# Optimization experiments

Hardware: AMD Instinct MI355X
Metric: run time of the kernel (lower is better)

Reference implementation:

```python
import jax, jax.numpy as jnp
import numpy as np

B, P, ENC = 128, 196, 2048
A, E, D, V, L = 512, 512, 512, 10000, 22


def setup_inputs() -> dict:
    key = jax.random.key(0)
    ks = jax.random.split(key, 24)
    rn = lambda k, shp, s=0.02: jax.random.normal(k, shp, dtype=jnp.float32) * s
    lengths = jnp.sort(jax.random.randint(ks[3], (B,), 2, L + 1))[::-1]
    lengths = lengths.at[0].set(L)  # ensure max_len = L-1 decode steps
    return {
        "encoder_out": jax.random.normal(ks[0], (B, P, ENC), dtype=jnp.float32),
        "encoded_captions": jax.random.randint(ks[1], (B, L), 0, V),
        "caption_lengths": lengths,
        "E_emb": rn(ks[2], (V, E)),
        "W_enc_att": rn(ks[4], (A, ENC)), "b_enc_att": jnp.zeros((A,), jnp.float32),
        "W_dec_att": rn(ks[5], (A, D)), "b_dec_att": jnp.zeros((A,), jnp.float32),
        "w_full": rn(ks[6], (1, A)), "b_full": jnp.zeros((1,), jnp.float32),
        "W_init_h": rn(ks[7], (D, ENC)), "b_init_h": jnp.zeros((D,), jnp.float32),
        "W_init_c": rn(ks[8], (D, ENC)), "b_init_c": jnp.zeros((D,), jnp.float32),
        "W_ih": rn(ks[9], (4 * D, E + ENC)), "b_ih": jnp.zeros((4 * D,), jnp.float32),
        "W_hh": rn(ks[10], (4 * D, D)), "b_hh": jnp.zeros((4 * D,), jnp.float32),
        "W_fc": rn(ks[11], (V, D)), "b_fc": jnp.zeros((V,), jnp.float32),
    }


def reference(encoder_out, encoded_captions, caption_lengths, E_emb,
              W_enc_att, b_enc_att, W_dec_att, b_dec_att, w_full, b_full,
              W_init_h, b_init_h, W_init_c, b_init_c,
              W_ih, b_ih, W_hh, b_hh, W_fc, b_fc):
    T = encoded_captions.shape[1] - 1  # max decode steps (static)
    dec_len = caption_lengths - 1
    mean_enc = encoder_out.mean(axis=1)  # [B, ENC]
    h0 = mean_enc @ W_init_h.T + b_init_h
    c0 = mean_enc @ W_init_c.T + b_init_c
    # encoder-side attention projection is constant across timesteps -> hoist
    att1 = jnp.einsum('bpe,ae->bpa', encoder_out, W_enc_att) + b_enc_att  # [B,P,A]
    embs = E_emb[encoded_captions]  # [B, L, E]

    def step(carry, xs):
        h, c = carry
        t, emb_t = xs  # emb_t: [B, E]
        att2 = h @ W_dec_att.T + b_dec_att  # [B, A]
        e = jnp.einsum('bpa,a->bp', jax.nn.relu(att1 + att2[:, None, :]), w_full[0]) + b_full[0]
        alpha = jax.nn.softmax(e, axis=1)  # [B, P]
        awe = jnp.einsum('bpe,bp->be', encoder_out, alpha)  # [B, ENC]
        x = jnp.concatenate([emb_t, awe], axis=1)  # [B, E+ENC]
        gates = x @ W_ih.T + b_ih + h @ W_hh.T + b_hh  # [B, 4D]
        i, f, g, o = jnp.split(gates, 4, axis=1)
        i, f, o = jax.nn.sigmoid(i), jax.nn.sigmoid(f), jax.nn.sigmoid(o)
        g = jnp.tanh(g)
        c_new = f * c + i * g
        h_new = o * jnp.tanh(c_new)
        active = (dec_len > t)[:, None]  # ragged trim -> mask
        h2 = jnp.where(active, h_new, h)
        c2 = jnp.where(active, c_new, c)
        pred = jnp.where(active, h_new @ W_fc.T + b_fc, 0.0)  # [B, V]
        al = jnp.where(active, alpha, 0.0)
        return (h2, c2), (pred, al)

    xs = (jnp.arange(T), jnp.swapaxes(embs[:, :T], 0, 1))
    (_, _), (preds, alphas) = jax.lax.scan(step, (h0, c0), xs)
    return jnp.swapaxes(preds, 0, 1), jnp.swapaxes(alphas, 0, 1)
```

## Files before the change

kernel.cpp:

```cpp
#include <hip/hip_runtime.h>
#include <hip/hip_bf16.h>

#define B_  128
#define P_  196
#define ENCD 2048
#define A_  512
#define E_  512
#define D_  512
#define V_  10000
#define L_  22
#define T_  21
#define VPAD 10112

typedef __attribute__((ext_vector_type(8))) short short8;
typedef __attribute__((ext_vector_type(4))) float f32x4;

static __device__ __forceinline__ float bf2f(unsigned short u){
  union { unsigned int i; float f; } x; x.i = ((unsigned int)u) << 16; return x.f;
}
static __device__ __forceinline__ unsigned short f2bf(float f){
  union { float f; unsigned int i; } x; x.f = f;
  unsigned int r = x.i + 0x7fffu + ((x.i >> 16) & 1u);
  return (unsigned short)(r >> 16);
}
static __device__ __forceinline__ unsigned int pack2(float a, float b){
  return (unsigned int)f2bf(a) | ((unsigned int)f2bf(b) << 16);
}
static __device__ __forceinline__ void glds16(const void* g, void* l){
  __builtin_amdgcn_global_load_lds((const __attribute__((address_space(1))) void*)g,
                                   (__attribute__((address_space(3))) void*)l, 16, 0, 0);
}

__global__ __launch_bounds__(256) void gemm128(
    const unsigned short* __restrict__ A, int lda,
    const unsigned short* __restrict__ B, int ldb, int K,
    const float* __restrict__ bias,
    float* __restrict__ outF, long ldo,
    unsigned short* __restrict__ outB, long ldob,
    int ntiles)
{
  __shared__ unsigned short As[2][128*32];
  __shared__ unsigned short Bs[2][128*32];
  int bid = blockIdx.x, nblk = gridDim.x;
  if ((nblk & 7) == 0){ int per = nblk >> 3; bid = (bid & 7)*per + (bid >> 3); }
  int nt = bid % ntiles, mt = bid / ntiles;
  int tid = threadIdx.x, wave = tid >> 6, lane = tid & 63;
  int quad = lane >> 4, l16 = lane & 15;

  const unsigned short* ga = A + (size_t)(mt*128 + wave*32 + (lane>>2))*lda + (lane&3)*8;
  const unsigned short* gb = B + (size_t)(nt*128 + wave*32 + (lane>>2))*ldb + (lane&3)*8;

  int wm = wave >> 1, wn = wave & 1;

  auto STAGE = [&](int buf, int kk){
    unsigned short* la = &As[buf][wave*1024];
    unsigned short* lb = &Bs[buf][wave*1024];
    glds16(ga + kk,                  la);
    glds16(ga + kk + (size_t)16*lda, la + 512);
    glds16(gb + kk,                  lb);
    glds16(gb + kk + (size_t)16*ldb, lb + 512);
  };

  f32x4 acc[4][4];
  #pragma unroll
  for (int i=0;i<4;++i)
    #pragma unroll
    for (int j=0;j<4;++j) acc[i][j] = (f32x4){0.f,0.f,0.f,0.f};

  STAGE(0, 0);
  int cur = 0;
  for (int k=0; k<K; k+=32){
    __syncthreads();
    if (k+32 < K) STAGE(cur^1, k+32);
    const unsigned short* rA = &As[cur][(wm*64 + l16)*32 + quad*8];
    const unsigned short* rB = &Bs[cur][(wn*64 + l16)*32 + quad*8];
    short8 af[4], bfr[4];
    #pragma unroll
    for (int i=0;i<4;++i) af[i]  = *(const short8*)(rA + i*16*32);
    #pragma unroll
    for (int i=0;i<4;++i) bfr[i] = *(const short8*)(rB + i*16*32);
    #pragma unroll
    for (int mf=0;mf<4;++mf)
      #pragma unroll
      for (int nf=0;nf<4;++nf)
        acc[mf][nf] = __builtin_amdgcn_mfma_f32_16x16x32_bf16(af[mf], bfr[nf], acc[mf][nf], 0,0,0);
    cur ^= 1;
  }

  #pragma unroll
  for (int mf=0;mf<4;++mf){
    long mbase = mt*128 + wm*64 + mf*16 + quad*4;
    #pragma unroll
    for (int nf=0;nf<4;++nf){
      int col = nt*128 + wn*64 + nf*16 + l16;
      float bv = bias ? bias[col] : 0.f;
      #pragma unroll
      for (int r=0;r<4;++r){
        float v = acc[mf][nf][r] + bv;
        long m = mbase + r;
        if (outF) outF[m*ldo + col] = v;
        if (outB) outB[m*ldob + col] = f2bf(v);
      }
    }
  }
}

__global__ __launch_bounds__(256) void gemm_preds(
    const unsigned short* __restrict__ A,
    const unsigned short* __restrict__ B,
    const float* __restrict__ bias,
    const int* __restrict__ rs,
    const int* __restrict__ trow, const int* __restrict__ brow,
    float* __restrict__ out)
{
  __shared__ unsigned short As[2][128*32];
  __shared__ unsigned short Bs[2][128*32];
  int nt = blockIdx.x % 79, mt = blockIdx.x / 79;
  int NR = rs[T_];
  if (mt*128 >= NR) return;
  int tid = threadIdx.x, wave = tid >> 6, lane = tid & 63;
  int quad = lane >> 4, l16 = lane & 15;

  const unsigned short* ga = A + (size_t)(mt*128 + wave*32 + (lane>>2))*D_ + (lane&3)*8;
  const unsigned short* gb = B + (size_t)(nt*128 + wave*32 + (lane>>2))*D_ + (lane&3)*8;

  int wm = wave >> 1, wn = wave & 1;

  auto STAGE = [&](int buf, int kk){
    unsigned short* la = &As[buf][wave*1024];
    unsigned short* lb = &Bs[buf][wave*1024];
    glds16(ga + kk,                 la);
    glds16(ga + kk + (size_t)16*D_, la + 512);
    glds16(gb + kk,                 lb);
    glds16(gb + kk + (size_t)16*D_, lb + 512);
  };

  f32x4 acc[4][4];
  #pragma unroll
  for (int i=0;i<4;++i)
    #pragma unroll
    for (int j=0;j<4;++j) acc[i][j] = (f32x4){0.f,0.f,0.f,0.f};

  STAGE(0, 0);
  int cur = 0;
  for (int k=0; k<D_; k+=32){
    __syncthreads();
    if (k+32 < D_) STAGE(cur^1, k+32);
    const unsigned short* rA = &As[cur][(wm*64 + l16)*32 + quad*8];
    const unsigned short* rB = &Bs[cur][(wn*64 + l16)*32 + quad*8];
    short8 af[4], bfr[4];
    #pragma unroll
    for (int i=0;i<4;++i) af[i]  = *(const short8*)(rA + i*16*32);
    #pragma unroll
    for (int i=0;i<4;++i) bfr[i] = *(const short8*)(rB + i*16*32);
    #pragma unroll
    for (int mf=0;mf<4;++mf)
      #pragma unroll
      for (int nf=0;nf<4;++nf)
        acc[mf][nf] = __builtin_amdgcn_mfma_f32_16x16x32_bf16(af[mf], bfr[nf], acc[mf][nf], 0,0,0);
    cur ^= 1;
  }

  #pragma unroll
  for (int mf=0;mf<4;++mf){
    int mbase = mt*128 + wm*64 + mf*16 + quad*4;
    #pragma unroll
    for (int nf=0;nf<4;++nf){
      int col = nt*128 + wn*64 + nf*16 + l16;
      if (col >= V_) continue;
      float bv = bias[col];
      #pragma unroll
      for (int r=0;r<4;++r){
        int row = mbase + r;
        if (row >= NR) continue;
        int tt = trow[row], bb = brow[row];
        out[(size_t)(bb*T_ + tt)*V_ + col] = acc[mf][nf][r] + bv;
      }
    }
  }
}

__global__ __launch_bounds__(512) void att_step(
    const float* __restrict__ h,
    const unsigned short* __restrict__ WdaT,
    const float* __restrict__ bda,
    const unsigned short* __restrict__ att1,
    const float* __restrict__ wfull, const float* __restrict__ bfull,
    const unsigned short* __restrict__ enc_bf,
    const int* __restrict__ actv, int t,
    unsigned short* __restrict__ awe_bf,
    float* __restrict__ out_alpha, long ldo)
{
  __shared__ float hs[D_];
  __shared__ float att2p[1024];
  __shared__ float att2s[A_];
  __shared__ float wfs[A_];
  __shared__ float als[256];
  __shared__ float red[16];

  int bid = blockIdx.x, tid = threadIdx.x;
  int wave = tid >> 6, lane = tid & 63;
  int b = bid >> 1, j = bid & 1;

  if (b >= actv[t]){
    if (j == 0 && tid < P_) out_alpha[(size_t)b*ldo + tid] = 0.f;
    return;
  }

  if (tid < 128){
    ((float4*)wfs)[tid] = ((const float4*)wfull)[tid];
    ((float4*)hs)[tid]  = ((const float4*)(h + (size_t)b*D_))[tid];
  }
  __syncthreads();

  {
    int half = tid >> 8, ap = tid & 255;
    const unsigned int* wp = (const unsigned int*)WdaT + (size_t)half*256*256 + ap;
    const float* hh = hs + half*256;
    float s0 = 0.f, s1 = 0.f;
    #pragma unroll 4
    for (int k=0;k<256;++k){
      unsigned int v = wp[(size_t)k*256];
      float hk = hh[k];
      s0 = fmaf(bf2f((unsigned short)(v & 0xffffu)), hk, s0);
      s1 = fmaf(bf2f((unsigned short)(v >> 16)),     hk, s1);
    }
    att2p[half*512 + ap*2]     = s0;
    att2p[half*512 + ap*2 + 1] = s1;
  }
  __syncthreads();
  if (tid < A_) att2s[tid] = att2p[tid] + att2p[512 + tid] + bda[tid];
  __syncthreads();

  for (int p = wave; p < P_; p += 8){
    short8 v = *(const short8*)(att1 + ((size_t)(b*P_ + p))*A_ + lane*8);
    float4 a20 = *(const float4*)(att2s + lane*8);
    float4 a21 = *(const float4*)(att2s + lane*8 + 4);
    float4 wf0 = *(const float4*)(wfs + lane*8);
    float4 wf1 = *(const float4*)(wfs + lane*8 + 4);
    float s = 0.f;
    s += fmaxf(bf2f((unsigned short)v[0]) + a20.x, 0.f) * wf0.x;
    s += fmaxf(bf2f((unsigned short)v[1]) + a20.y, 0.f) * wf0.y;
    s += fmaxf(bf2f((unsigned short)v[2]) + a20.z, 0.f) * wf0.z;
    s += fmaxf(bf2f((unsigned short)v[3]) + a20.w, 0.f) * wf0.w;
    s += fmaxf(bf2f((unsigned short)v[4]) + a21.x, 0.f) * wf1.x;
    s += fmaxf(bf2f((unsigned short)v[5]) + a21.y, 0.f) * wf1.y;
    s += fmaxf(bf2f((unsigned short)v[6]) + a21.z, 0.f) * wf1.z;
    s += fmaxf(bf2f((unsigned short)v[7]) + a21.w, 0.f) * wf1.w;
    #pragma unroll
    for (int off=32; off; off>>=1) s += __shfl_xor(s, off, 64);
    if (lane == 0) als[p] = s + bfull[0];
  }
  __syncthreads();

  float ev = (tid < P_) ? als[tid] : -1e30f;
  float mx = ev;
  #pragma unroll
  for (int off=32; off; off>>=1) mx = fmaxf(mx, __shfl_xor(mx, off, 64));
  if (lane == 0) red[wave] = mx;
  __syncthreads();
  float bmax = fmaxf(fmaxf(fmaxf(red[0],red[1]), fmaxf(red[2],red[3])),
                     fmaxf(fmaxf(red[4],red[5]), fmaxf(red[6],red[7])));
  float ex = (tid < P_) ? __expf(ev - bmax) : 0.f;
  float sm = ex;
  #pragma unroll
  for (int off=32; off; off>>=1) sm += __shfl_xor(sm, off, 64);
  if (lane == 0) red[8 + wave] = sm;
  __syncthreads();
  float inv = 1.f / (red[8]+red[9]+red[10]+red[11]+red[12]+red[13]+red[14]+red[15]);
  if (tid < P_){
    float alpha = ex * inv;
    als[tid] = alpha;
    if (j == 0) out_alpha[(size_t)b*ldo + tid] = alpha;
  }
  __syncthreads();

  {
    int cu = j*512 + tid;
    const unsigned int* ep = (const unsigned int*)enc_bf + (size_t)b*P_*1024 + cu;
    float a0 = 0.f, a1 = 0.f;
    for (int p=0; p<P_; p+=2){
      unsigned int v0 = ep[(size_t)(p+0)*1024];
      unsigned int v1 = ep[(size_t)(p+1)*1024];
      float x0 = als[p], x1 = als[p+1];
      a0 = fmaf(bf2f((unsigned short)(v0 & 0xffffu)), x0, a0);
      a1 = fmaf(bf2f((unsigned short)(v0 >> 16)),     x0, a1);
      a0 = fmaf(bf2f((unsigned short)(v1 & 0xffffu)), x1, a0);
      a1 = fmaf(bf2f((unsigned short)(v1 >> 16)),     x1, a1);
    }
    ((unsigned int*)awe_bf)[(size_t)b*1024 + cu] = pack2(a0, a1);
  }
}

__global__ __launch_bounds__(512) void gates_step(
    const unsigned short* __restrict__ hbf,
    const unsigned short* __restrict__ Whh,
    const unsigned short* __restrict__ awe,
    const unsigned short* __restrict__ Wienc,
    const float* __restrict__ gates_pre,
    float* __restrict__ h, float* __restrict__ c,
    unsigned short* __restrict__ hbf_out,
    unsigned short* __restrict__ h_cmp,
    const int* __restrict__ lens,
    const int* __restrict__ actv, const int* __restrict__ rs, int t)
{
  __shared__ float reds[8*1024];
  int bid = blockIdx.x;
  int nt = (bid & 7)*4 + ((bid >> 3) & 3);
  int mt = bid >> 5;
  int tid = threadIdx.x, wave = tid >> 6, lane = tid & 63;
  int quad = lane >> 4, l16 = lane & 15;
  int m0 = mt*16;
  int nact = actv[t];

  if (m0 >= nact){
    if (tid < 256){
      int mi = tid >> 4, di = tid & 15;
      int idx = (m0 + mi)*512 + nt*16 + di;
      hbf_out[idx] = hbf[idx];
    }
    return;
  }

  int ks = wave*320, ke = ks + 320;
  f32x4 acc[4];
  #pragma unroll
  for (int f=0;f<4;++f) acc[f] = (f32x4){0.f,0.f,0.f,0.f};

  for (int kk=ks; kk<ke; kk+=32){
    const unsigned short* Ap; const unsigned short* Bp; int k, lda2, ldb2;
    if (kk < 512){ Ap = hbf;  Bp = Whh;   k = kk;       lda2 = 512;  ldb2 = 512;  }
    else         { Ap = awe;  Bp = Wienc; k = kk - 512; lda2 = 2048; ldb2 = 2048; }
    short8 a = *(const short8*)(Ap + (size_t)(m0 + l16)*lda2 + k + quad*8);
    #pragma unroll
    for (int f=0;f<4;++f){
      short8 bb = *(const short8*)(Bp + (size_t)(nt*16 + f*512 + l16)*ldb2 + k + quad*8);
      acc[f] = __builtin_amdgcn_mfma_f32_16x16x32_bf16(a, bb, acc[f], 0,0,0);
    }
  }
  {
    float* dst = &reds[wave*1024 + lane*16];
    #pragma unroll
    for (int f=0;f<4;++f) ((f32x4*)dst)[f] = acc[f];
  }
  __syncthreads();
  if (tid < 256){
    int mi = tid >> 4, di = tid & 15;
    int m = m0 + mi, d = nt*16 + di;
    int rl = ((mi>>2)*16 + di)*16 + (mi&3);
    float g4[4];
    #pragma unroll
    for (int f=0;f<4;++f){
      float s = 0.f;
      #pragma unroll
      for (int w=0;w<8;++w) s += reds[w*1024 + rl + f*4];
      g4[f] = s;
    }
    const float* gp = gates_pre + ((size_t)m*T_ + t)*2048;
    float vi = g4[0] + gp[d];
    float vf = g4[1] + gp[512 + d];
    float vg = g4[2] + gp[1024 + d];
    float vo = g4[3] + gp[1536 + d];
    float si = 1.f/(1.f + __expf(-vi));
    float sf = 1.f/(1.f + __expf(-vf));
    float so = 1.f/(1.f + __expf(-vo));
    float tg = tanhf(vg);
    int idx = m*512 + d;
    float cn = sf*c[idx] + si*tg;
    float hn = so*tanhf(cn);
    bool act = m < nact;
    float h2 = act ? hn : h[idx];
    float c2 = act ? cn : c[idx];
    h[idx] = h2; c[idx] = c2;
    unsigned short hb = f2bf(h2);
    hbf_out[idx] = hb;
    if (act) h_cmp[(size_t)(rs[t] + m)*512 + d] = hb;
  }
}

__global__ __launch_bounds__(256) void calc_active(
    const int* __restrict__ lens, int* __restrict__ actv,
    int* __restrict__ rs, int* __restrict__ trow, int* __restrict__ brow)
{
  __shared__ int scnt[T_];
  __shared__ int srs[T_+1];
  int tid = threadIdx.x;
  if (tid < T_){
    int cnt = 0;
    for (int b=0;b<B_;++b) cnt += ((lens[b]-1) > tid) ? 1 : 0;
    scnt[tid] = cnt; actv[tid] = cnt;
  }
  __syncthreads();
  if (tid == 0){
    int s = 0;
    for (int t=0;t<T_;++t){ srs[t] = s; rs[t] = s; s += scnt[t]; }
    srs[T_] = s; rs[T_] = s;
  }
  __syncthreads();
  int NR = srs[T_];
  for (int r = tid; r < NR; r += 256){
    int t = 0;
    while (r >= srs[t+1]) ++t;
    trow[r] = t; brow[r] = r - srs[t];
  }
}

__global__ __launch_bounds__(256) void zero_inactive(
    const int* __restrict__ lens, float* __restrict__ out)
{
  int bid = blockIdx.x;
  int b = bid / T_, t = bid - b*T_;
  if ((lens[b]-1) > t) return;
  float4* o = (float4*)(out + (size_t)(b*T_ + t)*V_);
  float4 z = {0.f,0.f,0.f,0.f};
  for (int i = threadIdx.x; i < V_/4; i += 256) o[i] = z;
}

__global__ __launch_bounds__(256) void enc_cvt_mean(
    const float* __restrict__ enc, unsigned short* __restrict__ enc_bf,
    unsigned short* __restrict__ mean_bf)
{
  int b = blockIdx.x >> 1;
  int c = (blockIdx.x & 1)*1024 + threadIdx.x*4;
  size_t base = (size_t)b*P_*ENCD + c;
  float s0=0.f,s1=0.f,s2=0.f,s3=0.f;
  for (int p=0; p<P_; p+=2){
    float4 v0 = *(const float4*)(enc + base + (size_t)(p+0)*ENCD);
    float4 v1 = *(const float4*)(enc + base + (size_t)(p+1)*ENCD);
    s0 += v0.x + v1.x; s1 += v0.y + v1.y; s2 += v0.z + v1.z; s3 += v0.w + v1.w;
    uint2 r0; r0.x = pack2(v0.x, v0.y); r0.y = pack2(v0.z, v0.w);
    uint2 r1; r1.x = pack2(v1.x, v1.y); r1.y = pack2(v1.z, v1.w);
    *(uint2*)(enc_bf + base + (size_t)(p+0)*ENCD) = r0;
    *(uint2*)(enc_bf + base + (size_t)(p+1)*ENCD) = r1;
  }
  const float is = 1.f/196.f;
  uint2 m; m.x = pack2(s0*is, s1*is); m.y = pack2(s2*is, s3*is);
  *(uint2*)(mean_bf + (size_t)b*ENCD + c) = m;
}

__global__ __launch_bounds__(256) void cvt_bf16(
    const float* __restrict__ in, unsigned short* __restrict__ out, int n4)
{
  int i = blockIdx.x*256 + threadIdx.x;
  if (i < n4){
    float4 v = ((const float4*)in)[i];
    uint2 o; o.x = pack2(v.x, v.y); o.y = pack2(v.z, v.w);
    ((uint2*)out)[i] = o;
  }
}

__global__ __launch_bounds__(256) void cvt_T_512(
    const float* __restrict__ W, unsigned short* __restrict__ WT)
{
  int a = blockIdx.x;
  for (int k = threadIdx.x; k < 512; k += 256)
    WT[(size_t)k*512 + a] = f2bf(W[(size_t)a*512 + k]);
}

__global__ __launch_bounds__(256) void split_wih(
    const float* __restrict__ W, unsigned short* __restrict__ Wemb,
    unsigned short* __restrict__ Wenc)
{
  int j = blockIdx.x;
  for (int k4 = threadIdx.x; k4 < 640; k4 += 256){
    float4 v = *(const float4*)(W + (size_t)j*2560 + k4*4);
    uint2 o; o.x = pack2(v.x, v.y); o.y = pack2(v.z, v.w);
    if (k4 < 128) *(uint2*)(Wemb + (size_t)j*512  + k4*4)        = o;
    else          *(uint2*)(Wenc + (size_t)j*2048 + (k4-128)*4)  = o;
  }
}

__global__ void add_bias2(const float* __restrict__ a, const float* __restrict__ b,
                          float* __restrict__ out, int n)
{
  int i = blockIdx.x*256 + threadIdx.x;
  if (i < n) out[i] = a[i] + b[i];
}

__global__ __launch_bounds__(128) void gather_emb(
    const int* __restrict__ caps, const float* __restrict__ E,
    unsigned short* __restrict__ X)
{
  int r = blockIdx.x;
  int b = r / T_, t = r - b*T_;
  int tok = caps[b*L_ + t];
  int c = threadIdx.x*4;
  float4 v = *(const float4*)(E + (size_t)tok*E_ + c);
  uint2 o; o.x = pack2(v.x, v.y); o.y = pack2(v.z, v.w);
  *(uint2*)(X + (size_t)r*E_ + c) = o;
}

extern "C" void kernel_launch(void* const* d_in, const int* in_sizes, int n_in,
                              void* d_out, int out_size, void* d_ws, size_t ws_size,
                              hipStream_t stream)
{
  const float* enc   = (const float*)d_in[0];
  const int*   caps  = (const int*)d_in[1];
  const int*   lens  = (const int*)d_in[2];
  const float* Eemb  = (const float*)d_in[3];
  const float* Wea   = (const float*)d_in[4];
  const float* bea   = (const float*)d_in[5];
  const float* Wda   = (const float*)d_in[6];
  const float* bda   = (const float*)d_in[7];
  const float* wfull = (const float*)d_in[8];
  const float* bfull = (const float*)d_in[9];
  const float* Wih0  = (const float*)d_in[10];
  const float* bih0  = (const float*)d_in[11];
  const float* Wic0  = (const float*)d_in[12];
  const float* bic0  = (const float*)d_in[13];
  const float* Wih   = (const float*)d_in[14];
  const float* bih   = (const float*)d_in[15];
  const float* Whh   = (const float*)d_in[16];
  const float* bhh   = (const float*)d_in[17];
  const float* Wfc   = (const float*)d_in[18];
  const float* bfc   = (const float*)d_in[19];

  char* wsp = (char*)d_ws;
  auto carve = [&](size_t bytes) -> char* {
    char* p = wsp; wsp += (bytes + 255) & ~(size_t)255; return p;
  };
  unsigned short* enc_bf   = (unsigned short*)carve((size_t)B_*P_*ENCD*2);
  unsigned short* att1_bf  = (unsigned short*)carve((size_t)B_*P_*A_*2);
  unsigned short* mean_bf  = (unsigned short*)carve((size_t)B_*ENCD*2);
  float*          gates_pre= (float*)carve((size_t)B_*T_*2048*4);
  unsigned short* X_emb    = (unsigned short*)carve((size_t)B_*T_*E_*2);
  unsigned short* Wea_bf   = (unsigned short*)carve((size_t)A_*ENCD*2);
  unsigned short* WdaT_bf  = (unsigned short*)carve((size_t)A_*D_*2);
  unsigned short* Wh0_bf   = (unsigned short*)carve((size_t)D_*ENCD*2);
  unsigned short* Wc0_bf   = (unsigned short*)carve((size_t)D_*ENCD*2);
  unsigned short* Whh_bf   = (unsigned short*)carve((size_t)2048*D_*2);
  unsigned short* Wie_bf   = (unsigned short*)carve((size_t)2048*E_*2);
  unsigned short* Wienc_bf = (unsigned short*)carve((size_t)2048*ENCD*2);
  unsigned short* Wfc_bf   = (unsigned short*)carve((size_t)VPAD*D_*2);
  float*          bias_ifgo= (float*)carve((size_t)2048*4);
  float*          h        = (float*)carve((size_t)B_*D_*4);
  float*          c        = (float*)carve((size_t)B_*D_*4);
  unsigned short* h_bf_all = (unsigned short*)carve((size_t)(T_+1)*B_*D_*2);
  unsigned short* h_cmp    = (unsigned short*)carve((size_t)T_*B_*D_*2);
  unsigned short* awe_bf   = (unsigned short*)carve((size_t)B_*ENCD*2);
  int*            actv     = (int*)carve(64*4);
  int*            rs       = (int*)carve(64*4);
  int*            trow     = (int*)carve((size_t)T_*B_*4);
  int*            brow     = (int*)carve((size_t)T_*B_*4);

  float* out_preds  = (float*)d_out;
  float* out_alphas = (float*)d_out + (size_t)B_*T_*V_;

  calc_active<<<1, 256, 0, stream>>>(lens, actv, rs, trow, brow);
  zero_inactive<<<B_*T_, 256, 0, stream>>>(lens, out_preds);
  enc_cvt_mean<<<256, 256, 0, stream>>>(enc, enc_bf, mean_bf);
  cvt_bf16<<<1024, 256, 0, stream>>>(Wea,  Wea_bf, A_*ENCD/4);
  cvt_T_512<<<512, 256, 0, stream>>>(Wda, WdaT_bf);
  cvt_bf16<<<1024, 256, 0, stream>>>(Wih0, Wh0_bf, D_*ENCD/4);
  cvt_bf16<<<1024, 256, 0, stream>>>(Wic0, Wc0_bf, D_*ENCD/4);
  cvt_bf16<<<1024, 256, 0, stream>>>(Whh,  Whh_bf, 2048*D_/4);
  cvt_bf16<<<5000, 256, 0, stream>>>(Wfc,  Wfc_bf, V_*D_/4);
  split_wih<<<2048, 256, 0, stream>>>(Wih, Wie_bf, Wienc_bf);
  add_bias2<<<8, 256, 0, stream>>>(bih, bhh, bias_ifgo, 2048);
  gather_emb<<<B_*T_, 128, 0, stream>>>(caps, Eemb, X_emb);

  gemm128<<<1*4, 256, 0, stream>>>(mean_bf, ENCD, Wh0_bf, ENCD, ENCD,
                                   bih0, h, D_, h_bf_all, D_, 4);
  gemm128<<<1*4, 256, 0, stream>>>(mean_bf, ENCD, Wc0_bf, ENCD, ENCD,
                                   bic0, c, D_, (unsigned short*)0, 0, 4);
  gemm128<<<196*4, 256, 0, stream>>>(enc_bf, ENCD, Wea_bf, ENCD, ENCD,
                                     bea, (float*)0, 0, att1_bf, A_, 4);
  gemm128<<<21*16, 256, 0, stream>>>(X_emb, E_, Wie_bf, E_, E_,
                                     bias_ifgo, gates_pre, 2048, (unsigned short*)0, 0, 16);

  for (int t = 0; t < T_; ++t){
    att_step<<<2*B_, 512, 0, stream>>>(h, WdaT_bf, bda, att1_bf, wfull, bfull,
                                       enc_bf, actv, t, awe_bf,
                                       out_alphas + (size_t)t*P_, (long)T_*P_);
    gates_step<<<256, 512, 0, stream>>>(h_bf_all + (size_t)t*B_*D_, Whh_bf,
                                        awe_bf, Wienc_bf, gates_pre,
                                        h, c, h_bf_all + (size_t)(t+1)*B_*D_,
                                        h_cmp, lens, actv, rs, t);
  }

  gemm_preds<<<21*79, 256, 0, stream>>>(h_cmp, Wfc_bf, bfc, rs, trow, brow,
                                        out_preds);
}
```

Measured before the change: 1.954 ms.

## Fuse per-step attention and gate kernels into one persistent kernel with grid barriers

Replaces the 42 per-timestep launches of att_step and gates_step with a single persistent kernel of 256 blocks. The blocks loop over timesteps and use an atomic-counter grid barrier between the attention phase and the gate phase. This removes kernel launch overhead and inter-kernel gaps. It relies on all 256 blocks being co-resident, since the barrier deadlocks otherwise. It also adds spin-wait cost and a larger shared-memory footprint per block, which may lower occupancy.

```diff
diff --git a/kernel.cpp b/kernel.cpp
--- a/kernel.cpp
+++ b/kernel.cpp
@@ -11,6 +11,7 @@
 #define L_  22
 #define T_  21
 #define VPAD 10112
+#define NBLK 256
 
 typedef __attribute__((ext_vector_type(8))) short short8;
 typedef __attribute__((ext_vector_type(4))) float f32x4;
@@ -29,6 +30,18 @@
 static __device__ __forceinline__ void glds16(const void* g, void* l){
   __builtin_amdgcn_global_load_lds((const __attribute__((address_space(1))) void*)g,
                                    (__attribute__((address_space(3))) void*)l, 16, 0, 0);
+}
+
+static __device__ __forceinline__ void gridbar(int* cnt, int target){
+  __syncthreads();
+  if (threadIdx.x == 0){
+    __threadfence();
+    __hip_atomic_fetch_add(cnt, 1, __ATOMIC_ACQ_REL, __HIP_MEMORY_SCOPE_AGENT);
+    while (__hip_atomic_load(cnt, __ATOMIC_ACQUIRE, __HIP_MEMORY_SCOPE_AGENT) < target)
+      __builtin_amdgcn_s_sleep(2);
+    __threadfence();
+  }
+  __syncthreads();
 }
 
 __global__ __launch_bounds__(256) void gemm128(
@@ -180,16 +193,23 @@
   }
 }
 
-__global__ __launch_bounds__(512) void att_step(
-    const float* __restrict__ h,
+__global__ __launch_bounds__(512) void decode_persist(
+    float* __restrict__ h,
     const unsigned short* __restrict__ WdaT,
     const float* __restrict__ bda,
     const unsigned short* __restrict__ att1,
     const float* __restrict__ wfull, const float* __restrict__ bfull,
     const unsigned short* __restrict__ enc_bf,
-    const int* __restrict__ actv, int t,
+    const unsigned short* __restrict__ Whh,
+    const unsigned short* __restrict__ Wienc,
+    const float* __restrict__ gates_pre,
+    float* __restrict__ c,
+    unsigned short* __restrict__ h_bf_all,
+    unsigned short* __restrict__ h_cmp,
     unsigned short* __restrict__ awe_bf,
-    float* __restrict__ out_alpha, long ldo)
+    const int* __restrict__ actv, const int* __restrict__ rs,
+    float* __restrict__ out_alphas,
+    int* __restrict__ barcnt)
 {
   __shared__ float hs[D_];
   __shared__ float att2p[1024];
@@ -197,194 +217,191 @@
   __shared__ float wfs[A_];
   __shared__ float als[256];
   __shared__ float red[16];
+  __shared__ float reds[8*1024];
 
   int bid = blockIdx.x, tid = threadIdx.x;
   int wave = tid >> 6, lane = tid & 63;
+  int quad = lane >> 4, l16 = lane & 15;
   int b = bid >> 1, j = bid & 1;
-
-  if (b >= actv[t]){
-    if (j == 0 && tid < P_) out_alpha[(size_t)b*ldo + tid] = 0.f;
-    return;
-  }
-
-  if (tid < 128){
-    ((float4*)wfs)[tid] = ((const float4*)wfull)[tid];
-    ((float4*)hs)[tid]  = ((const float4*)(h + (size_t)b*D_))[tid];
-  }
-  __syncthreads();
-
-  {
-    int half = tid >> 8, ap = tid & 255;
-    const unsigned int* wp = (const unsigned int*)WdaT + (size_t)half*256*256 + ap;
-    const float* hh = hs + half*256;
-    float s0 = 0.f, s1 = 0.f;
-    #pragma unroll 4
-    for (int k=0;k<256;++k){
-      unsigned int v = wp[(size_t)k*256];
-      float hk = hh[k];
-      s0 = fmaf(bf2f((unsigned short)(v & 0xffffu)), hk, s0);
-      s1 = fmaf(bf2f((unsigned short)(v >> 16)),     hk, s1);
+  int ntg = (bid & 7)*4 + ((bid >> 3) & 3);
+  int mtg = bid >> 5;
+  int m0 = mtg*16;
+  int target = 0;
+
+  if (tid < 128) ((float4*)wfs)[tid] = ((const float4*)wfull)[tid];
+  float bf0 = bfull[0];
+
+  for (int t = 0; t < T_; ++t){
+    int nact = actv[t];
+    float* out_alpha = out_alphas + (size_t)t*P_;
+
+    if (b < nact){
+      if (tid < 128) ((float4*)hs)[tid] = ((const float4*)(h + (size_t)b*D_))[tid];
+      __syncthreads();
+
+      {
+        int half = tid >> 8, ap = tid & 255;
+        const unsigned int* wp = (const unsigned int*)WdaT + (size_t)half*256*256 + ap;
+        const float* hh = hs + half*256;
+        float s0 = 0.f, s1 = 0.f;
+        #pragma unroll 4
+        for (int k=0;k<256;++k){
+          unsigned int v = wp[(size_t)k*256];
+          float hk = hh[k];
+          s0 = fmaf(bf2f((unsigned short)(v & 0xffffu)), hk, s0);
+          s1 = fmaf(bf2f((unsigned short)(v >> 16)),     hk, s1);
+        }
+        att2p[half*512 + ap*2]     = s0;
+        att2p[half*512 + ap*2 + 1] = s1;
+      }
+      __syncthreads();
+      if (tid < A_) att2s[tid] = att2p[tid] + att2p[512 + tid] + bda[tid];
+      __syncthreads();
+
+      for (int p = wave; p < P_; p += 8){
+        short8 v = *(const short8*)(att1 + ((size_t)(b*P_ + p))*A_ + lane*8);
+        float4 a20 = *(const float4*)(att2s + lane*8);
+        float4 a21 = *(const float4*)(att2s + lane*8 + 4);
+        float4 wf0 = *(const float4*)(wfs + lane*8);
+        float4 wf1 = *(const float4*)(wfs + lane*8 + 4);
+        float s = 0.f;
+        s += fmaxf(bf2f((unsigned short)v[0]) + a20.x, 0.f) * wf0.x;
+        s += fmaxf(bf2f((unsigned short)v[1]) + a20.y, 0.f) * wf0.y;
+        s += fmaxf(bf2f((unsigned short)v[2]) + a20.z, 0.f) * wf0.z;
+        s += fmaxf(bf2f((unsigned short)v[3]) + a20.w, 0.f) * wf0.w;
+        s += fmaxf(bf2f((unsigned short)v[4]) + a21.x, 0.f) * wf1.x;
+        s += fmaxf(bf2f((unsigned short)v[5]) + a21.y, 0.f) * wf1.y;
+        s += fmaxf(bf2f((unsigned short)v[6]) + a21.z, 0.f) * wf1.z;
+        s += fmaxf(bf2f((unsigned short)v[7]) + a21.w, 0.f) * wf1.w;
+        #pragma unroll
+        for (int off=32; off; off>>=1) s += __shfl_xor(s, off, 64);
+        if (lane == 0) als[p] = s + bf0;
+      }
+      __syncthreads();
+
+      float ev = (tid < P_) ? als[tid] : -1e30f;
+      float mx = ev;
+      #pragma unroll
+      for (int off=32; off; off>>=1) mx = fmaxf(mx, __shfl_xor(mx, off, 64));
+      if (lane == 0) red[wave] = mx;
+      __syncthreads();
+      float bmax = fmaxf(fmaxf(fmaxf(red[0],red[1]), fmaxf(red[2],red[3])),
+                         fmaxf(fmaxf(red[4],red[5]), fmaxf(red[6],red[7])));
+      float ex = (tid < P_) ? __expf(ev - bmax) : 0.f;
+      float sm = ex;
+      #pragma unroll
+      for (int off=32; off; off>>=1) sm += __shfl_xor(sm, off, 64);
+      if (lane == 0) red[8 + wave] = sm;
+      __syncthreads();
+      float inv = 1.f / (red[8]+red[9]+red[10]+red[11]+red[12]+red[13]+red[14]+red[15]);
+      if (tid < P_){
+        float alpha = ex * inv;
+        als[tid] = alpha;
+        if (j == 0) out_alpha[(size_t)b*(T_*(long)P_) + tid] = alpha;
+      }
+      __syncthreads();
+
+      {
+        int cu = j*512 + tid;
+        const unsigned int* ep = (const unsigned int*)enc_bf + (size_t)b*P_*1024 + cu;
+        float a0 = 0.f, a1 = 0.f;
+        for (int p=0; p<P_; p+=2){
+          unsigned int v0 = ep[(size_t)(p+0)*1024];
+          unsigned int v1 = ep[(size_t)(p+1)*1024];
+          float x0 = als[p], x1 = als[p+1];
+          a0 = fmaf(bf2f((unsigned short)(v0 & 0xffffu)), x0, a0);
+          a1 = fmaf(bf2f((unsigned short)(v0 >> 16)),     x0, a1);
+          a0 = fmaf(bf2f((unsigned short)(v1 & 0xffffu)), x1, a0);
+          a1 = fmaf(bf2f((unsigned short)(v1 >> 16)),     x1, a1);
+        }
+        ((unsigned int*)awe_bf)[(size_t)b*1024 + cu] = pack2(a0, a1);
+      }
+    } else {
+      if (j == 0 && tid < P_) out_alpha[(size_t)b*(T_*(long)P_) + tid] = 0.f;
     }
-    att2p[half*512 + ap*2]     = s0;
-    att2p[half*512 + ap*2 + 1] = s1;
-  }
-  __syncthreads();
-  if (tid < A_) att2s[tid] = att2p[tid] + att2p[512 + tid] + bda[tid];
-  __syncthreads();
-
-  for (int p = wave; p < P_; p += 8){
-    short8 v = *(const short8*)(att1 + ((size_t)(b*P_ + p))*A_ + lane*8);
-    float4 a20 = *(const float4*)(att2s + lane*8);
-    float4 a21 = *(const float4*)(att2s + lane*8 + 4);
-    float4 wf0 = *(const float4*)(wfs + lane*8);
-    float4 wf1 = *(const float4*)(wfs + lane*8 + 4);
-    float s = 0.f;
-    s += fmaxf(bf2f((unsigned short)v[0]) + a20.x, 0.f) * wf0.x;
-    s += fmaxf(bf2f((unsigned short)v[1]) + a20.y, 0.f) * wf0.y;
-    s += fmaxf(bf2f((unsigned short)v[2]) + a20.z, 0.f) * wf0.z;
-    s += fmaxf(bf2f((unsigned short)v[3]) + a20.w, 0.f) * wf0.w;
-    s += fmaxf(bf2f((unsigned short)v[4]) + a21.x, 0.f) * wf1.x;
-    s += fmaxf(bf2f((unsigned short)v[5]) + a21.y, 0.f) * wf1.y;
-    s += fmaxf(bf2f((unsigned short)v[6]) + a21.z, 0.f) * wf1.z;
-    s += fmaxf(bf2f((unsigned short)v[7]) + a21.w, 0.f) * wf1.w;
-    #pragma unroll
-    for (int off=32; off; off>>=1) s += __shfl_xor(s, off, 64);
-    if (lane == 0) als[p] = s + bfull[0];
-  }
-  __syncthreads();
-
-  float ev = (tid < P_) ? als[tid] : -1e30f;
-  float mx = ev;
-  #pragma unroll
-  for (int off=32; off; off>>=1) mx = fmaxf(mx, __shfl_xor(mx, off, 64));
-  if (lane == 0) red[wave] = mx;
-  __syncthreads();
-  float bmax = fmaxf(fmaxf(fmaxf(red[0],red[1]), fmaxf(red[2],red[3])),
-                     fmaxf(fmaxf(red[4],red[5]), fmaxf(red[6],red[7])));
-  float ex = (tid < P_) ? __expf(ev - bmax) : 0.f;
-  float sm = ex;
-  #pragma unroll
-  for (int off=32; off; off>>=1) sm += __shfl_xor(sm, off, 64);
-  if (lane == 0) red[8 + wave] = sm;
-  __syncthreads();
-  float inv = 1.f / (red[8]+red[9]+red[10]+red[11]+red[12]+red[13]+red[14]+red[15]);
-  if (tid < P_){
-    float alpha = ex * inv;
-    als[tid] = alpha;
-    if (j == 0) out_alpha[(size_t)b*ldo + tid] = alpha;
-  }
-  __syncthreads();
-
-  {
-    int cu = j*512 + tid;
-    const unsigned int* ep = (const unsigned int*)enc_bf + (size_t)b*P_*1024 + cu;
-    float a0 = 0.f, a1 = 0.f;
-    for (int p=0; p<P_; p+=2){
-      unsigned int v0 = ep[(size_t)(p+0)*1024];
-      unsigned int v1 = ep[(size_t)(p+1)*1024];
-      float x0 = als[p], x1 = als[p+1];
-      a0 = fmaf(bf2f((unsigned short)(v0 & 0xffffu)), x0, a0);
-      a1 = fmaf(bf2f((unsigned short)(v0 >> 16)),     x0, a1);
-      a0 = fmaf(bf2f((unsigned short)(v1 & 0xffffu)), x1, a0);
-      a1 = fmaf(bf2f((unsigned short)(v1 >> 16)),     x1, a1);
+
+    target += NBLK; gridbar(barcnt, target);
+
+    const unsigned short* hbf = h_bf_all + (size_t)t*B_*D_;
+    unsigned short* hbf_out   = h_bf_all + (size_t)(t+1)*B_*D_;
+
+    if (m0 >= nact){
+      if (tid < 256){
+        int mi = tid >> 4, di = tid & 15;
+        int idx = (m0 + mi)*512 + ntg*16 + di;
+        hbf_out[idx] = hbf[idx];
+      }
+    } else {
+      int ks = wave*320, ke = ks + 320;
+      f32x4 acc[4];
+      #pragma unroll
+      for (int f=0;f<4;++f) acc[f] = (f32x4){0.f,0.f,0.f,0.f};
+
+      for (int kk=ks; kk<ke; kk+=32){
+        const unsigned short* Ap; const unsigned short* Bp; int k, lda2, ldb2;
+        if (kk < 512){ Ap = hbf;    Bp = Whh;   k = kk;       lda2 = 512;  ldb2 = 512;  }
+        else         { Ap = awe_bf; Bp = Wienc; k = kk - 512; lda2 = 2048; ldb2 = 2048; }
+        short8 a = *(const short8*)(Ap + (size_t)(m0 + l16)*lda2 + k + quad*8);
+        #pragma unroll
+        for (int f=0;f<4;++f){
+          short8 bb = *(const short8*)(Bp + (size_t)(ntg*16 + f*512 + l16)*ldb2 + k + quad*8);
+          acc[f] = __builtin_amdgcn_mfma_f32_16x16x32_bf16(a, bb, acc[f], 0,0,0);
+        }
+      }
+      {
+        float* dst = &reds[wave*1024 + lane*16];
+        #pragma unroll
+        for (int f=0;f<4;++f) ((f32x4*)dst)[f] = acc[f];
+      }
+      __syncthreads();
+      if (tid < 256){
+        int mi = tid >> 4, di = tid & 15;
+        int m = m0 + mi, d = ntg*16 + di;
+        int rl = ((mi>>2)*16 + di)*16 + (mi&3);
+        float g4[4];
+        #pragma unroll
+        for (int f=0;f<4;++f){
+          float s = 0.f;
+          #pragma unroll
+          for (int w=0;w<8;++w) s += reds[w*1024 + rl + f*4];
+          g4[f] = s;
+        }
+        const float* gp = gates_pre + ((size_t)m*T_ + t)*2048;
+        float vi = g4[0] + gp[d];
+        float vf = g4[1] + gp[512 + d];
+        float vg = g4[2] + gp[1024 + d];
+        float vo = g4[3] + gp[1536 + d];
+        float si = 1.f/(1.f + __expf(-vi));
+        float sf = 1.f/(1.f + __expf(-vf));
+        float so = 1.f/(1.f + __expf(-vo));
+        float tg = tanhf(vg);
+        int idx = m*512 + d;
+        float cn = sf*c[idx] + si*tg;
+        float hn = so*tanhf(cn);
+        bool act = m < nact;
+        float h2 = act ? hn : h[idx];
+        float c2 = act ? cn : c[idx];
+        h[idx] = h2; c[idx] = c2;
+        unsigned short hb = f2bf(h2);
+        hbf_out[idx] = hb;
+        if (act) h_cmp[(size_t)(rs[t] + m)*512 + d] = hb;
+      }
+      __syncthreads();
     }
-    ((unsigned int*)awe_bf)[(size_t)b*1024 + cu] = pack2(a0, a1);
-  }
-}
-
-__global__ __launch_bounds__(512) void gates_step(
-    const unsigned short* __restrict__ hbf,
-    const unsigned short* __restrict__ Whh,
-    const unsigned short* __restrict__ awe,
-    const unsigned short* __restrict__ Wienc,
-    const float* __restrict__ gates_pre,
-    float* __restrict__ h, float* __restrict__ c,
-    unsigned short* __restrict__ hbf_out,
-    unsigned short* __restrict__ h_cmp,
-    const int* __restrict__ lens,
-    const int* __restrict__ actv, const int* __restrict__ rs, int t)
-{
-  __shared__ float reds[8*1024];
-  int bid = blockIdx.x;
-  int nt = (bid & 7)*4 + ((bid >> 3) & 3);
-  int mt = bid >> 5;
-  int tid = threadIdx.x, wave = tid >> 6, lane = tid & 63;
-  int quad = lane >> 4, l16 = lane & 15;
-  int m0 = mt*16;
-  int nact = actv[t];
-
-  if (m0 >= nact){
-    if (tid < 256){
-      int mi = tid >> 4, di = tid & 15;
-      int idx = (m0 + mi)*512 + nt*16 + di;
-      hbf_out[idx] = hbf[idx];
-    }
-    return;
-  }
-
-  int ks = wave*320, ke = ks + 320;
-  f32x4 acc[4];
-  #pragma unroll
-  for (int f=0;f<4;++f) acc[f] = (f32x4){0.f,0.f,0.f,0.f};
-
-  for (int kk=ks; kk<ke; kk+=32){
-    const unsigned short* Ap; const unsigned short* Bp; int k, lda2, ldb2;
-    if (kk < 512){ Ap = hbf;  Bp = Whh;   k = kk;       lda2 = 512;  ldb2 = 512;  }
-    else         { Ap = awe;  Bp = Wienc; k = kk - 512; lda2 = 2048; ldb2 = 2048; }
-    short8 a = *(const short8*)(Ap + (size_t)(m0 + l16)*lda2 + k + quad*8);
-    #pragma unroll
-    for (int f=0;f<4;++f){
-      short8 bb = *(const short8*)(Bp + (size_t)(nt*16 + f*512 + l16)*ldb2 + k + quad*8);
-      acc[f] = __builtin_amdgcn_mfma_f32_16x16x32_bf16(a, bb, acc[f], 0,0,0);
-    }
-  }
-  {
-    float* dst = &reds[wave*1024 + lane*16];
-    #pragma unroll
-    for (int f=0;f<4;++f) ((f32x4*)dst)[f] = acc[f];
-  }
-  __syncthreads();
-  if (tid < 256){
-    int mi = tid >> 4, di = tid & 15;
-    int m = m0 + mi, d = nt*16 + di;
-    int rl = ((mi>>2)*16 + di)*16 + (mi&3);
-    float g4[4];
-    #pragma unroll
-    for (int f=0;f<4;++f){
-      float s = 0.f;
-      #pragma unroll
-      for (int w=0;w<8;++w) s += reds[w*1024 + rl + f*4];
-      g4[f] = s;
-    }
-    const float* gp = gates_pre + ((size_t)m*T_ + t)*2048;
-    float vi = g4[0] + gp[d];
-    float vf = g4[1] + gp[512 + d];
-    float vg = g4[2] + gp[1024 + d];
-    float vo = g4[3] + gp[1536 + d];
-    float si = 1.f/(1.f + __expf(-vi));
-    float sf = 1.f/(1.f + __expf(-vf));
-    float so = 1.f/(1.f + __expf(-vo));
-    float tg = tanhf(vg);
-    int idx = m*512 + d;
-    float cn = sf*c[idx] + si*tg;
-    float hn = so*tanhf(cn);
-    bool act = m < nact;
-    float h2 = act ? hn : h[idx];
-    float c2 = act ? cn : c[idx];
-    h[idx] = h2; c[idx] = c2;
-    unsigned short hb = f2bf(h2);
-    hbf_out[idx] = hb;
-    if (act) h_cmp[(size_t)(rs[t] + m)*512 + d] = hb;
+
+    target += NBLK; gridbar(barcnt, target);
   }
 }
 
 __global__ __launch_bounds__(256) void calc_active(
     const int* __restrict__ lens, int* __restrict__ actv,
-    int* __restrict__ rs, int* __restrict__ trow, int* __restrict__ brow)
+    int* __restrict__ rs, int* __restrict__ trow, int* __restrict__ brow,
+    int* __restrict__ barcnt)
 {
   __shared__ int scnt[T_];
   __shared__ int srs[T_+1];
   int tid = threadIdx.x;
+  if (tid == 0) barcnt[0] = 0;
   if (tid < T_){
     int cnt = 0;
     for (int b=0;b<B_;++b) cnt += ((lens[b]-1) > tid) ? 1 : 0;
@@ -542,11 +559,12 @@
   int*            rs       = (int*)carve(64*4);
   int*            trow     = (int*)carve((size_t)T_*B_*4);
   int*            brow     = (int*)carve((size_t)T_*B_*4);
+  int*            barcnt   = (int*)carve(256);
 
   float* out_preds  = (float*)d_out;
   float* out_alphas = (float*)d_out + (size_t)B_*T_*V_;
 
-  calc_active<<<1, 256, 0, stream>>>(lens, actv, rs, trow, brow);
+  calc_active<<<1, 256, 0, stream>>>(lens, actv, rs, trow, brow, barcnt);
   zero_inactive<<<B_*T_, 256, 0, stream>>>(lens, out_preds);
   enc_cvt_mean<<<256, 256, 0, stream>>>(enc, enc_bf, mean_bf);
   cvt_bf16<<<1024, 256, 0, stream>>>(Wea,  Wea_bf, A_*ENCD/4);
@@ -568,15 +586,10 @@
   gemm128<<<21*16, 256, 0, stream>>>(X_emb, E_, Wie_bf, E_, E_,
                                      bias_ifgo, gates_pre, 2048, (unsigned short*)0, 0, 16);
 
-  for (int t = 0; t < T_; ++t){
-    att_step<<<2*B_, 512, 0, stream>>>(h, WdaT_bf, bda, att1_bf, wfull, bfull,
-                                       enc_bf, actv, t, awe_bf,
-                                       out_alphas + (size_t)t*P_, (long)T_*P_);
-    gates_step<<<256, 512, 0, stream>>>(h_bf_all + (size_t)t*B_*D_, Whh_bf,
-                                        awe_bf, Wienc_bf, gates_pre,
-                                        h, c, h_bf_all + (size_t)(t+1)*B_*D_,
-                                        h_cmp, lens, actv, rs, t);
-  }
+  decode_persist<<<NBLK, 512, 0, stream>>>(
+      h, WdaT_bf, bda, att1_bf, wfull, bfull, enc_bf,
+      Whh_bf, Wienc_bf, gates_pre, c, h_bf_all, h_cmp, awe_bf,
+      actv, rs, out_alphas, barcnt);
 
   gemm_preds<<<21*79, 256, 0, stream>>>(h_cmp, Wfc_bf, bfc, rs, trow, brow,
                                         out_preds);
```

Result: slower. 4.999 ms (+155.9%).

## Triple-buffer GEMM staging, widen attention-weighted sum loads, split gates K loop

Applied to the files above, without the earlier changes.

Both bf16 GEMM kernels move from double to triple buffered LDS staging. They prefetch two K-tiles ahead and use explicit vmcnt waits plus a raw s_barrier in place of __syncthreads. The attention kernel's weighted encoder sum now uses 16-byte loads with eight outputs per thread, splits P across four thread groups and reduces the partials through shared memory, and unrolls the att2 matvec further. The gates kernel splits its K loop into separate h·Whh and awe·Wienc loops so the per-iteration pointer selection goes away. The cost is more LDS use, which may lower occupancy, and reliance on the hand-counted vmcnt being correct.

```diff
diff --git a/kernel.cpp b/kernel.cpp
--- a/kernel.cpp
+++ b/kernel.cpp
@@ -39,8 +39,8 @@
     unsigned short* __restrict__ outB, long ldob,
     int ntiles)
 {
-  __shared__ unsigned short As[2][128*32];
-  __shared__ unsigned short Bs[2][128*32];
+  __shared__ unsigned short As[3][128*32];
+  __shared__ unsigned short Bs[3][128*32];
   int bid = blockIdx.x, nblk = gridDim.x;
   if ((nblk & 7) == 0){ int per = nblk >> 3; bid = (bid & 7)*per + (bid >> 3); }
   int nt = bid % ntiles, mt = bid / ntiles;
@@ -68,10 +68,14 @@
     for (int j=0;j<4;++j) acc[i][j] = (f32x4){0.f,0.f,0.f,0.f};
 
   STAGE(0, 0);
+  STAGE(1, 32);
   int cur = 0;
   for (int k=0; k<K; k+=32){
-    __syncthreads();
-    if (k+32 < K) STAGE(cur^1, k+32);
+    if (k+32 < K) asm volatile("s_waitcnt vmcnt(4)" ::: "memory");
+    else          asm volatile("s_waitcnt vmcnt(0)" ::: "memory");
+    __builtin_amdgcn_s_barrier();
+    __builtin_amdgcn_sched_barrier(0);
+    if (k+64 < K) STAGE(cur==0 ? 2 : (cur==1 ? 0 : 1), k+64);
     const unsigned short* rA = &As[cur][(wm*64 + l16)*32 + quad*8];
     const unsigned short* rB = &Bs[cur][(wn*64 + l16)*32 + quad*8];
     short8 af[4], bfr[4];
@@ -84,7 +88,7 @@
       #pragma unroll
       for (int nf=0;nf<4;++nf)
         acc[mf][nf] = __builtin_amdgcn_mfma_f32_16x16x32_bf16(af[mf], bfr[nf], acc[mf][nf], 0,0,0);
-    cur ^= 1;
+    cur = (cur==2) ? 0 : cur+1;
   }
 
   #pragma unroll
@@ -113,8 +117,8 @@
     const int* __restrict__ trow, const int* __restrict__ brow,
     float* __restrict__ out)
 {
-  __shared__ unsigned short As[2][128*32];
-  __shared__ unsigned short Bs[2][128*32];
+  __shared__ unsigned short As[3][128*32];
+  __shared__ unsigned short Bs[3][128*32];
   int nt = blockIdx.x % 79, mt = blockIdx.x / 79;
   int NR = rs[T_];
   if (mt*128 >= NR) return;
@@ -142,10 +146,14 @@
     for (int j=0;j<4;++j) acc[i][j] = (f32x4){0.f,0.f,0.f,0.f};
 
   STAGE(0, 0);
+  STAGE(1, 32);
   int cur = 0;
   for (int k=0; k<D_; k+=32){
-    __syncthreads();
-    if (k+32 < D_) STAGE(cur^1, k+32);
+    if (k+32 < D_) asm volatile("s_waitcnt vmcnt(4)" ::: "memory");
+    else           asm volatile("s_waitcnt vmcnt(0)" ::: "memory");
+    __builtin_amdgcn_s_barrier();
+    __builtin_amdgcn_sched_barrier(0);
+    if (k+64 < D_) STAGE(cur==0 ? 2 : (cur==1 ? 0 : 1), k+64);
     const unsigned short* rA = &As[cur][(wm*64 + l16)*32 + quad*8];
     const unsigned short* rB = &Bs[cur][(wn*64 + l16)*32 + quad*8];
     short8 af[4], bfr[4];
@@ -158,7 +166,7 @@
       #pragma unroll
       for (int nf=0;nf<4;++nf)
         acc[mf][nf] = __builtin_amdgcn_mfma_f32_16x16x32_bf16(af[mf], bfr[nf], acc[mf][nf], 0,0,0);
-    cur ^= 1;
+    cur = (cur==2) ? 0 : cur+1;
   }
 
   #pragma unroll
@@ -197,6 +205,7 @@
   __shared__ float wfs[A_];
   __shared__ float als[256];
   __shared__ float red[16];
+  __shared__ float awred[3*1160];
 
   int bid = blockIdx.x, tid = threadIdx.x;
   int wave = tid >> 6, lane = tid & 63;
@@ -218,7 +227,7 @@
     const unsigned int* wp = (const unsigned int*)WdaT + (size_t)half*256*256 + ap;
     const float* hh = hs + half*256;
     float s0 = 0.f, s1 = 0.f;
-    #pragma unroll 4
+    #pragma unroll 16
     for (int k=0;k<256;++k){
       unsigned int v = wp[(size_t)k*256];
       float hk = hh[k];
@@ -276,19 +285,45 @@
   __syncthreads();
 
   {
-    int cu = j*512 + tid;
-    const unsigned int* ep = (const unsigned int*)enc_bf + (size_t)b*P_*1024 + cu;
-    float a0 = 0.f, a1 = 0.f;
-    for (int p=0; p<P_; p+=2){
-      unsigned int v0 = ep[(size_t)(p+0)*1024];
-      unsigned int v1 = ep[(size_t)(p+1)*1024];
-      float x0 = als[p], x1 = als[p+1];
-      a0 = fmaf(bf2f((unsigned short)(v0 & 0xffffu)), x0, a0);
-      a1 = fmaf(bf2f((unsigned short)(v0 >> 16)),     x0, a1);
-      a0 = fmaf(bf2f((unsigned short)(v1 & 0xffffu)), x1, a0);
-      a1 = fmaf(bf2f((unsigned short)(v1 >> 16)),     x1, a1);
-    }
-    ((unsigned int*)awe_bf)[(size_t)b*1024 + cu] = pack2(a0, a1);
+    int sub = tid >> 7, ti = tid & 127;
+    const uint4* ep = (const uint4*)enc_bf + (size_t)b*P_*256 + j*128 + ti;
+    float a8[8];
+    #pragma unroll
+    for (int i=0;i<8;++i) a8[i] = 0.f;
+    #pragma unroll 8
+    for (int pp=0; pp<49; ++pp){
+      int p = sub + pp*4;
+      uint4 v = ep[(size_t)p*256];
+      float al = als[p];
+      a8[0] = fmaf(bf2f((unsigned short)(v.x & 0xffffu)), al, a8[0]);
+      a8[1] = fmaf(bf2f((unsigned short)(v.x >> 16)),     al, a8[1]);
+      a8[2] = fmaf(bf2f((unsigned short)(v.y & 0xffffu)), al, a8[2]);
+      a8[3] = fmaf(bf2f((unsigned short)(v.y >> 16)),     al, a8[3]);
+      a8[4] = fmaf(bf2f((unsigned short)(v.z & 0xffffu)), al, a8[4]);
+      a8[5] = fmaf(bf2f((unsigned short)(v.z >> 16)),     al, a8[5]);
+      a8[6] = fmaf(bf2f((unsigned short)(v.w & 0xffffu)), al, a8[6]);
+      a8[7] = fmaf(bf2f((unsigned short)(v.w >> 16)),     al, a8[7]);
+    }
+    if (sub > 0){
+      float* dst = &awred[(sub-1)*1160 + ti*9];
+      #pragma unroll
+      for (int i=0;i<8;++i) dst[i] = a8[i];
+    }
+    __syncthreads();
+    if (sub == 0){
+      #pragma unroll
+      for (int w=0;w<3;++w){
+        const float* src = &awred[w*1160 + ti*9];
+        #pragma unroll
+        for (int i=0;i<8;++i) a8[i] += src[i];
+      }
+      uint4 o;
+      o.x = pack2(a8[0], a8[1]);
+      o.y = pack2(a8[2], a8[3]);
+      o.z = pack2(a8[4], a8[5]);
+      o.w = pack2(a8[6], a8[7]);
+      ((uint4*)awe_bf)[(size_t)b*256 + j*128 + ti] = o;
+    }
   }
 }
 
@@ -327,17 +362,28 @@
   #pragma unroll
   for (int f=0;f<4;++f) acc[f] = (f32x4){0.f,0.f,0.f,0.f};
 
-  for (int kk=ks; kk<ke; kk+=32){
-    const unsigned short* Ap; const unsigned short* Bp; int k, lda2, ldb2;
-    if (kk < 512){ Ap = hbf;  Bp = Whh;   k = kk;       lda2 = 512;  ldb2 = 512;  }
-    else         { Ap = awe;  Bp = Wienc; k = kk - 512; lda2 = 2048; ldb2 = 2048; }
-    short8 a = *(const short8*)(Ap + (size_t)(m0 + l16)*lda2 + k + quad*8);
+  int e1 = ke < 512 ? ke : 512;
+  #pragma unroll 2
+  for (int kk=ks; kk<e1; kk+=32){
+    short8 a = *(const short8*)(hbf + (size_t)(m0 + l16)*512 + kk + quad*8);
     #pragma unroll
     for (int f=0;f<4;++f){
-      short8 bb = *(const short8*)(Bp + (size_t)(nt*16 + f*512 + l16)*ldb2 + k + quad*8);
+      short8 bb = *(const short8*)(Whh + (size_t)(nt*16 + f*512 + l16)*512 + kk + quad*8);
       acc[f] = __builtin_amdgcn_mfma_f32_16x16x32_bf16(a, bb, acc[f], 0,0,0);
     }
   }
+  int s2 = ks > 512 ? ks - 512 : 0;
+  int e2 = ke - 512;
+  #pragma unroll 2
+  for (int k=s2; k<e2; k+=32){
+    short8 a = *(const short8*)(awe + (size_t)(m0 + l16)*2048 + k + quad*8);
+    #pragma unroll
+    for (int f=0;f<4;++f){
+      short8 bb = *(const short8*)(Wienc + (size_t)(nt*16 + f*512 + l16)*2048 + k + quad*8);
+      acc[f] = __builtin_amdgcn_mfma_f32_16x16x32_bf16(a, bb, acc[f], 0,0,0);
+    }
+  }
+
   {
     float* dst = &reds[wave*1024 + lane*16];
     #pragma unroll
```

After: 1.724 ms. -11.7%, faster.
